# Optimization experiments

Measured on AMD Instinct MI355X. Metric: run time of the kernel, lower is better.

Reference implementation:

```python
import jax, jax.numpy as jnp
import numpy as np

SPATIAL_SHAPES = np.array([[128, 128], [64, 64], [32, 32], [16, 16]], dtype=np.int32)  # (H, W) per level
D_MODEL = 256
D_FFN = 1024
N_LEVELS = 4
N_HEADS = 8
N_POINTS = 4
HEAD_DIM = D_MODEL // N_HEADS
B = 2
LEN = int((SPATIAL_SHAPES[:, 0] * SPATIAL_SHAPES[:, 1]).sum())  # 21760


def layer_norm(x, g, b, eps=1e-5):
    mu = x.mean(-1, keepdims=True)
    var = ((x - mu) ** 2).mean(-1, keepdims=True)
    return (x - mu) / jnp.sqrt(var + eps) * g + b


def ms_deform_attn_core(value, sampling_locations, attention_weights):
    # value: [B, Len, M, D]; locations: [B, Lq, M, L, P, 2] in [0,1]; weights: [B, Lq, M, L, P]
    B_, _, M, D = value.shape
    Lq = sampling_locations.shape[1]
    P = sampling_locations.shape[4]
    out = jnp.zeros((B_, M, Lq, D), value.dtype)
    start = 0
    for lvl, (H, W) in enumerate(SPATIAL_SHAPES.tolist()):
        v = value[:, start:start + H * W].transpose(0, 2, 1, 3)  # [B, M, H*W, D]
        start += H * W
        loc = sampling_locations[:, :, :, lvl].transpose(0, 2, 1, 3, 4)  # [B, M, Lq, P, 2]
        # grid_sample semantics: align_corners=False, padding_mode='zeros'
        x = loc[..., 0] * W - 0.5
        y = loc[..., 1] * H - 0.5
        x0 = jnp.floor(x)
        y0 = jnp.floor(y)
        wx = (x - x0)[..., None]
        wy = (y - y0)[..., None]

        def gather(xi, yi):
            valid = ((xi >= 0) & (xi < W) & (yi >= 0) & (yi < H)).astype(value.dtype)
            idx = (jnp.clip(yi, 0, H - 1) * W + jnp.clip(xi, 0, W - 1)).astype(jnp.int32)
            idx = idx.reshape(B_, M, Lq * P)
            g = jnp.take_along_axis(v, idx[..., None], axis=2).reshape(B_, M, Lq, P, D)
            return g * valid[..., None]

        v00 = gather(x0, y0)
        v01 = gather(x0 + 1, y0)
        v10 = gather(x0, y0 + 1)
        v11 = gather(x0 + 1, y0 + 1)
        samp = (v00 * (1 - wx) + v01 * wx) * (1 - wy) + (v10 * (1 - wx) + v11 * wx) * wy
        w_l = attention_weights[:, :, :, lvl].transpose(0, 2, 1, 3)  # [B, M, Lq, P]
        out = out + (samp * w_l[..., None]).sum(axis=3)
    return out.transpose(0, 2, 1, 3).reshape(B_, Lq, M * D)


def setup_inputs() -> dict:
    key = jax.random.key(0)
    ks = jax.random.split(key, 16)
    f32 = jnp.float32

    def lin(k, fan_in, fan_out, scale=None):
        s = scale if scale is not None else 1.0 / np.sqrt(fan_in)
        return jax.random.normal(k, (fan_in, fan_out), f32) * s

    starts = np.concatenate([[0], np.cumsum(SPATIAL_SHAPES[:, 0] * SPATIAL_SHAPES[:, 1])[:-1]]).astype(np.int32)
    inp = {
        "src": jax.random.normal(ks[0], (B, LEN, D_MODEL), f32),
        "pos": jax.random.normal(ks[1], (B, LEN, D_MODEL), f32),
        "reference_points": jax.random.uniform(ks[2], (B, LEN, N_LEVELS, 2), f32),
        "spatial_shapes": jnp.asarray(SPATIAL_SHAPES),
        "level_start_index": jnp.asarray(starts),
        "norm1_g": jnp.ones((D_MODEL,), f32), "norm1_b": jnp.zeros((D_MODEL,), f32),
        "norm2_g": jnp.ones((D_MODEL,), f32), "norm2_b": jnp.zeros((D_MODEL,), f32),
        "W_value": lin(ks[3], D_MODEL, D_MODEL), "b_value": jnp.zeros((D_MODEL,), f32),
        "W_off": lin(ks[4], D_MODEL, N_HEADS * N_LEVELS * N_POINTS * 2, scale=0.01),
        "b_off": jax.random.normal(ks[5], (N_HEADS * N_LEVELS * N_POINTS * 2,), f32) * 0.01,
        "W_attn": lin(ks[6], D_MODEL, N_HEADS * N_LEVELS * N_POINTS),
        "b_attn": jnp.zeros((N_HEADS * N_LEVELS * N_POINTS,), f32),
        "W_out": lin(ks[7], D_MODEL, D_MODEL), "b_out": jnp.zeros((D_MODEL,), f32),
        "W_ffn1": lin(ks[8], D_MODEL, D_FFN), "b_ffn1": jnp.zeros((D_FFN,), f32),
        "W_ffn2": lin(ks[9], D_FFN, D_MODEL), "b_ffn2": jnp.zeros((D_MODEL,), f32),
    }
    return inp


def reference(src, pos, reference_points, spatial_shapes, level_start_index,
              norm1_g, norm1_b, norm2_g, norm2_b,
              W_value, b_value, W_off, b_off, W_attn, b_attn, W_out, b_out,
              W_ffn1, b_ffn1, W_ffn2, b_ffn2):
    B_, Lq, C = src.shape
    # pre-norm deformable self-attention; NOTE: value path uses un-normed src (faithful to source)
    q = layer_norm(src, norm1_g, norm1_b) + pos
    value = (src @ W_value + b_value).reshape(B_, Lq, N_HEADS, HEAD_DIM)
    offsets = (q @ W_off + b_off).reshape(B_, Lq, N_HEADS, N_LEVELS, N_POINTS, 2)
    attn = jax.nn.softmax((q @ W_attn + b_attn).reshape(B_, Lq, N_HEADS, N_LEVELS * N_POINTS), axis=-1)
    attn = attn.reshape(B_, Lq, N_HEADS, N_LEVELS, N_POINTS)
    offset_normalizer = spatial_shapes[..., ::-1].astype(src.dtype)  # (W, H) per level
    loc = reference_points[:, :, None, :, None, :] + offsets / offset_normalizer[None, None, None, :, None, :]
    attn_out = ms_deform_attn_core(value, loc, attn) @ W_out + b_out
    src = src + attn_out
    h = layer_norm(src, norm2_g, norm2_b)
    h = jax.nn.gelu(h @ W_ffn1 + b_ffn1, approximate=False) @ W_ffn2 + b_ffn2
    return src + h
```

## Files before the change

### kernel.cpp

```cpp
#include <hip/hip_runtime.h>
#include <hip/hip_bf16.h>
#include <math.h>

#define LEN_TOT 21760
#define BATCH 2
#define MROWS (BATCH * LEN_TOT)
#define DMODEL 256
#define DFFN 1024

typedef unsigned short ushort_t;
typedef __attribute__((ext_vector_type(8))) short short8;
typedef __attribute__((ext_vector_type(4))) float floatx4;
typedef __attribute__((address_space(3))) ushort_t lds_us;
typedef __attribute__((address_space(1))) const ushort_t glb_us;

__device__ __forceinline__ ushort_t f2b(float f) {
    unsigned u = __float_as_uint(f);
    unsigned r = (u + 0x7FFFu + ((u >> 16) & 1u)) >> 16;
    return (ushort_t)r;
}

struct TP {
    const float* s[6];
    ushort_t*    d[6];
    int K[6];
    int N[6];
    int start[7];
};

__global__ __launch_bounds__(256) void transpose_convert(TP tp) {
    __shared__ float tile[32][33];
    int blk = blockIdx.x;
    int seg = 0;
    while (seg < 5 && blk >= tp.start[seg + 1]) seg++;
    int local = blk - tp.start[seg];
    int K = tp.K[seg], N = tp.N[seg];
    int tn = N >> 5;
    int k0 = (local / tn) << 5, n0 = (local % tn) << 5;
    int r = threadIdx.x >> 5, c = threadIdx.x & 31;
    const float* src = tp.s[seg];
    #pragma unroll
    for (int rr = r; rr < 32; rr += 8)
        tile[rr][c] = src[(size_t)(k0 + rr) * N + n0 + c];
    __syncthreads();
    ushort_t* dst = tp.d[seg];
    #pragma unroll
    for (int rr = r; rr < 32; rr += 8)
        dst[(size_t)(n0 + rr) * K + k0 + c] = f2b(tile[c][rr]);
}

__global__ void bias_cat(const float* __restrict__ a, const float* __restrict__ b,
                         float* __restrict__ o) {
    int t = threadIdx.x;
    o[t] = (t < 256) ? a[t] : b[t - 256];
}

__global__ __launch_bounds__(256) void ln_dual_kernel(
    const float* __restrict__ x, const float* __restrict__ g,
    const float* __restrict__ bb, const float* __restrict__ addv,
    ushort_t* __restrict__ y_bf, ushort_t* __restrict__ x_bf)
{
    int row  = blockIdx.x * 4 + (threadIdx.x >> 6);
    int lane = threadIdx.x & 63;
    size_t base = (size_t)row * DMODEL + lane * 4;
    float4 v = *(const float4*)(x + base);

    float s = v.x + v.y + v.z + v.w;
    #pragma unroll
    for (int o = 32; o; o >>= 1) s += __shfl_xor(s, o, 64);
    float mu = s * (1.0f / 256.0f);

    float d0 = v.x - mu, d1 = v.y - mu, d2 = v.z - mu, d3 = v.w - mu;
    float vs = d0*d0 + d1*d1 + d2*d2 + d3*d3;
    #pragma unroll
    for (int o = 32; o; o >>= 1) vs += __shfl_xor(vs, o, 64);
    float rstd = rsqrtf(vs * (1.0f / 256.0f) + 1e-5f);

    float4 gv = *(const float4*)(g  + lane * 4);
    float4 bv = *(const float4*)(bb + lane * 4);
    float o0 = d0 * rstd * gv.x + bv.x;
    float o1 = d1 * rstd * gv.y + bv.y;
    float o2 = d2 * rstd * gv.z + bv.z;
    float o3 = d3 * rstd * gv.w + bv.w;
    if (addv) {
        float4 av = *(const float4*)(addv + base);
        o0 += av.x; o1 += av.y; o2 += av.z; o3 += av.w;
    }
    ushort4 ob = {f2b(o0), f2b(o1), f2b(o2), f2b(o3)};
    *(ushort4*)(y_bf + base) = ob;
    if (x_bf) {
        ushort4 xb = {f2b(v.x), f2b(v.y), f2b(v.z), f2b(v.w)};
        *(ushort4*)(x_bf + base) = xb;
    }
}

template<int GELU_ACT, int HAS_RES, int OUT_BF16>
__global__ __launch_bounds__(256) void gemm_mfma(
    const ushort_t* __restrict__ A, const ushort_t* __restrict__ Bt,
    const float* __restrict__ bias, const float* __restrict__ res,
    float* __restrict__ C, ushort_t* __restrict__ Cbf,
    int M, int N, int K)
{
    constexpr int BM = 128, BK = 64;
    __shared__ __align__(16) ushort_t As[BM * BK];
    __shared__ __align__(16) ushort_t Bs[BM * BK];

    const int tid  = threadIdx.x;
    const int wave = tid >> 6;
    const int lane = tid & 63;
    const int wm = (wave & 1) * 64;
    const int wn = (wave >> 1) * 64;
    const int ml = lane & 15;
    const int quad = lane >> 4;
    const int m0 = blockIdx.y * BM, n0 = blockIdx.x * BM;
    const int swz = ml & 7;

    floatx4 acc[4][4] = {};

    for (int k0 = 0; k0 < K; k0 += BK) {
        #pragma unroll
        for (int p = 0; p < 4; p++) {
            int c = p * 256 + tid;
            int r = c >> 3, sp = c & 7;
            int sl = sp ^ (r & 7);
            __builtin_amdgcn_global_load_lds(
                (glb_us*)(A + (size_t)(m0 + r) * K + k0 + sl * 8),
                (lds_us*)(As + c * 8), 16, 0, 0);
            __builtin_amdgcn_global_load_lds(
                (glb_us*)(Bt + (size_t)(n0 + r) * K + k0 + sl * 8),
                (lds_us*)(Bs + c * 8), 16, 0, 0);
        }
        __syncthreads();

        #pragma unroll
        for (int kb = 0; kb < 2; kb++) {
            const int sA = quad + 4 * kb;
            short8 af[4], bfr[4];
            #pragma unroll
            for (int i = 0; i < 4; i++)
                af[i] = *(const short8*)(As + (wm + i * 16 + ml) * BK + (sA ^ swz) * 8);
            #pragma unroll
            for (int j = 0; j < 4; j++)
                bfr[j] = *(const short8*)(Bs + (wn + j * 16 + ml) * BK + (sA ^ swz) * 8);
            #pragma unroll
            for (int i = 0; i < 4; i++)
                #pragma unroll
                for (int j = 0; j < 4; j++)
                    acc[i][j] = __builtin_amdgcn_mfma_f32_16x16x32_bf16(
                        af[i], bfr[j], acc[i][j], 0, 0, 0);
        }
        __syncthreads();
    }

    if (OUT_BF16) {
        ushort_t* pool  = (wave < 2) ? As : Bs;
        ushort_t* wbase = pool + (wave & 1) * 2048;
        const int lr  = lane >> 2;
        const int sg  = lane & 3;
        #pragma unroll
        for (int i = 0; i < 4; i++) {
            ushort_t* wbuf = wbase + (i & 1) * 1024;
            #pragma unroll
            for (int j = 0; j < 4; j++) {
                float bc = bias[n0 + wn + j * 16 + ml];
                #pragma unroll
                for (int r = 0; r < 4; r++) {
                    float v = acc[i][j][r] + bc;
                    if (GELU_ACT) v = 0.5f * v * (1.0f + erff(v * 0.7071067811865476f));
                    if (HAS_RES)
                        v += res[(size_t)(m0 + wm + i * 16 + quad * 4 + r) * N
                                 + n0 + wn + j * 16 + ml];
                    wbuf[(quad * 4 + r) * 64 + j * 16 + ml] = f2b(v);
                }
            }
            asm volatile("s_waitcnt lgkmcnt(0)" ::: "memory");
            #pragma unroll
            for (int h = 0; h < 2; h++) {
                short8 vv = *(const short8*)(wbuf + lr * 64 + (sg + 4 * h) * 8);
                *(short8*)(Cbf + (size_t)(m0 + wm + i * 16 + lr) * N
                                 + n0 + wn + (sg + 4 * h) * 8) = vv;
            }
        }
    } else {
        #pragma unroll
        for (int j = 0; j < 4; j++) {
            int col = n0 + wn + j * 16 + ml;
            float bc = bias[col];
            #pragma unroll
            for (int i = 0; i < 4; i++) {
                int row = m0 + wm + i * 16 + quad * 4;
                #pragma unroll
                for (int r = 0; r < 4; r++) {
                    float v = acc[i][j][r] + bc;
                    if (GELU_ACT) v = 0.5f * v * (1.0f + erff(v * 0.7071067811865476f));
                    if (HAS_RES) v += res[(size_t)(row + r) * N + col];
                    C[(size_t)(row + r) * N + col] = v;
                }
            }
        }
    }
}

__global__ __launch_bounds__(256) void msdeform_kernel(
    const ushort_t* __restrict__ value, const float* __restrict__ qk,
    const float* __restrict__ refp, ushort_t* __restrict__ out_bf)
{
    __shared__ int2 meta[8][16][4];

    const int t  = threadIdx.x;
    const int bq = blockIdx.x;
    const int b  = (bq >= LEN_TOT) ? 1 : 0;

    if (t < 128) {
        int g = t >> 4, i = t & 15;
        float logit = qk[(size_t)bq * 384 + 256 + g * 16 + i];
        float mx = logit;
        #pragma unroll
        for (int o = 8; o; o >>= 1) mx = fmaxf(mx, __shfl_xor(mx, o, 16));
        float e = __expf(logit - mx);
        float se = e;
        #pragma unroll
        for (int o = 8; o; o >>= 1) se += __shfl_xor(se, o, 16);
        float prob = e / se;

        int lvl = i >> 2;
        int Wl  = 128 >> lvl;
        float Wf = (float)Wl;
        const int ST_[4] = {0, 16384, 20480, 21504};

        float2 off2 = *(const float2*)(qk + (size_t)bq * 384 + g * 32 + i * 2);
        float2 ref2 = ((const float2*)refp)[(size_t)bq * 4 + lvl];
        float xs = fmaf(ref2.x, Wf, off2.x) - 0.5f;
        float ys = fmaf(ref2.y, Wf, off2.y) - 0.5f;
        float xf = floorf(xs), yf = floorf(ys);
        int x0 = (int)xf, y0 = (int)yf;
        float wx = xs - xf, wy = ys - yf;
        float wx1 = 1.0f - wx, wy1 = 1.0f - wy;

        bool vx0 = (x0 >= 0) & (x0 < Wl);
        bool vx1 = (x0 + 1 >= 0) & (x0 + 1 < Wl);
        bool vy0 = (y0 >= 0) & (y0 < Wl);
        bool vy1 = (y0 + 1 >= 0) & (y0 + 1 < Wl);
        int cx0 = min(max(x0, 0), Wl - 1);
        int cx1 = min(max(x0 + 1, 0), Wl - 1);
        int cy0 = min(max(y0, 0), Wl - 1);
        int cy1 = min(max(y0 + 1, 0), Wl - 1);

        int vbase = b * LEN_TOT + ST_[lvl];
        int i00 = (vbase + cy0 * Wl + cx0) * 256 + g * 32;
        int i01 = (vbase + cy0 * Wl + cx1) * 256 + g * 32;
        int i10 = (vbase + cy1 * Wl + cx0) * 256 + g * 32;
        int i11 = (vbase + cy1 * Wl + cx1) * 256 + g * 32;
        float w00 = (vx0 && vy0) ? prob * wx1 * wy1 : 0.0f;
        float w01 = (vx1 && vy0) ? prob * wx  * wy1 : 0.0f;
        float w10 = (vx0 && vy1) ? prob * wx1 * wy  : 0.0f;
        float w11 = (vx1 && vy1) ? prob * wx  * wy  : 0.0f;

        *(int4*)&meta[g][i][0] = make_int4(i00, __float_as_int(w00),
                                           i01, __float_as_int(w01));
        *(int4*)&meta[g][i][2] = make_int4(i10, __float_as_int(w10),
                                           i11, __float_as_int(w11));
    }
    __syncthreads();

    const int g  = t >> 5;
    const int l  = t & 31;
    const int cl = l >> 3;
    const int d4 = l & 7;
    float ax = 0.0f, ay = 0.0f, az = 0.0f, aw = 0.0f;
    #pragma unroll
    for (int s = 0; s < 16; s++) {
        int2 mw = meta[g][s][cl];
        float w = __int_as_float(mw.y);
        uint2 u = *(const uint2*)(value + mw.x + (d4 << 2));
        float f0 = __uint_as_float(u.x << 16);
        float f1 = __uint_as_float(u.x & 0xFFFF0000u);
        float f2 = __uint_as_float(u.y << 16);
        float f3 = __uint_as_float(u.y & 0xFFFF0000u);
        ax = fmaf(w, f0, ax); ay = fmaf(w, f1, ay);
        az = fmaf(w, f2, az); aw = fmaf(w, f3, aw);
    }
    ax += __shfl_xor(ax, 8, 32);  ay += __shfl_xor(ay, 8, 32);
    az += __shfl_xor(az, 8, 32);  aw += __shfl_xor(aw, 8, 32);
    ax += __shfl_xor(ax, 16, 32); ay += __shfl_xor(ay, 16, 32);
    az += __shfl_xor(az, 16, 32); aw += __shfl_xor(aw, 16, 32);

    if (l < 8) {
        ushort4 o = {f2b(ax), f2b(ay), f2b(az), f2b(aw)};
        *(ushort4*)(out_bf + ((size_t)bq * 8 + g) * 32 + (d4 << 2)) = o;
    }
}

extern "C" void kernel_launch(void* const* d_in, const int* in_sizes, int n_in,
                              void* d_out, int out_size, void* d_ws, size_t ws_size,
                              hipStream_t stream)
{
    const float* src  = (const float*)d_in[0];
    const float* pos  = (const float*)d_in[1];
    const float* refp = (const float*)d_in[2];
    const float* n1g = (const float*)d_in[5];
    const float* n1b = (const float*)d_in[6];
    const float* n2g = (const float*)d_in[7];
    const float* n2b = (const float*)d_in[8];
    const float* Wv  = (const float*)d_in[9];
    const float* bv  = (const float*)d_in[10];
    const float* Wof = (const float*)d_in[11];
    const float* bof = (const float*)d_in[12];
    const float* Wat = (const float*)d_in[13];
    const float* bat = (const float*)d_in[14];
    const float* Wo  = (const float*)d_in[15];
    const float* bo  = (const float*)d_in[16];
    const float* Wf1 = (const float*)d_in[17];
    const float* bf1 = (const float*)d_in[18];
    const float* Wf2 = (const float*)d_in[19];
    const float* bf2 = (const float*)d_in[20];
    float* out = (float*)d_out;

    char* ws = (char*)d_ws;
    const int M  = MROWS;
    const int Mc = M / 2;
    const size_t SZ_BF = (size_t)M * 256 * 2;

    ushort_t* q_bf     = (ushort_t*)(ws);
    ushort_t* src_bf   = (ushort_t*)(ws + SZ_BF);
    ushort_t* value_bf = (ushort_t*)(ws + 2 * SZ_BF);
    float*    qkb      = (float*)   (ws + 3 * SZ_BF);
    float*    src2     = (float*)   (ws + 4 * SZ_BF);
    ushort_t* h0_bf    = q_bf;
    ushort_t* sampled  = src_bf;
    ushort_t* h1_bf    = value_bf;
    char* wtp = ws + 3 * SZ_BF + (size_t)M * 384 * 4;
    ushort_t* WvT  = (ushort_t*)(wtp);
    ushort_t* WofT = WvT  + 256 * 256;
    ushort_t* WatT = WofT + 256 * 256;
    ushort_t* WoT  = WatT + 256 * 128;
    ushort_t* Wf1T = WoT  + 256 * 256;
    ushort_t* Wf2T = Wf1T + 256 * 1024;
    float*    bqk  = (float*)(Wf2T + 1024 * 256);

    TP tp;
    tp.s[0] = Wv;  tp.d[0] = WvT;  tp.K[0] = 256;  tp.N[0] = 256;
    tp.s[1] = Wof; tp.d[1] = WofT; tp.K[1] = 256;  tp.N[1] = 256;
    tp.s[2] = Wat; tp.d[2] = WatT; tp.K[2] = 256;  tp.N[2] = 128;
    tp.s[3] = Wo;  tp.d[3] = WoT;  tp.K[3] = 256;  tp.N[3] = 256;
    tp.s[4] = Wf1; tp.d[4] = Wf1T; tp.K[4] = 256;  tp.N[4] = 1024;
    tp.s[5] = Wf2; tp.d[5] = Wf2T; tp.K[5] = 1024; tp.N[5] = 256;
    tp.start[0] = 0;   tp.start[1] = 64;  tp.start[2] = 128;
    tp.start[3] = 160; tp.start[4] = 224; tp.start[5] = 480; tp.start[6] = 736;
    transpose_convert<<<736, 256, 0, stream>>>(tp);
    bias_cat<<<1, 384, 0, stream>>>(bof, bat, bqk);

    ln_dual_kernel<<<M / 4, 256, 0, stream>>>(src, n1g, n1b, pos, q_bf, src_bf);
    gemm_mfma<0, 0, 1><<<dim3(2, M / 128), 256, 0, stream>>>(
        src_bf, WvT, bv, nullptr, nullptr, value_bf, M, 256, 256);
    gemm_mfma<0, 0, 0><<<dim3(3, M / 128), 256, 0, stream>>>(
        q_bf, WofT, bqk, nullptr, qkb, nullptr, M, 384, 256);
    msdeform_kernel<<<M, 256, 0, stream>>>(value_bf, qkb, refp, sampled);
    gemm_mfma<0, 1, 0><<<dim3(2, M / 128), 256, 0, stream>>>(
        sampled, WoT, bo, src, src2, nullptr, M, 256, 256);
    ln_dual_kernel<<<M / 4, 256, 0, stream>>>(src2, n2g, n2b, nullptr, h0_bf, nullptr);
    for (int c = 0; c < 2; c++) {
        const ushort_t* h0c = h0_bf + (size_t)c * Mc * 256;
        const float*    s2c = src2  + (size_t)c * Mc * 256;
        float*          oc  = out   + (size_t)c * Mc * 256;
        gemm_mfma<1, 0, 1><<<dim3(8, Mc / 128), 256, 0, stream>>>(
            h0c, Wf1T, bf1, nullptr, nullptr, h1_bf, Mc, 1024, 256);
        gemm_mfma<0, 1, 0><<<dim3(2, Mc / 128), 256, 0, stream>>>(
            h1_bf, Wf2T, bf2, s2c, oc, nullptr, Mc, 256, 1024);
    }
}
```

Measured before the change: 505.4 us.

## Load GEMM fragments directly from global memory and process two queries per deform block

```diff
diff --git a/kernel.cpp b/kernel.cpp
--- a/kernel.cpp
+++ b/kernel.cpp
@@ -11,8 +11,6 @@
 typedef unsigned short ushort_t;
 typedef __attribute__((ext_vector_type(8))) short short8;
 typedef __attribute__((ext_vector_type(4))) float floatx4;
-typedef __attribute__((address_space(3))) ushort_t lds_us;
-typedef __attribute__((address_space(1))) const ushort_t glb_us;
 
 __device__ __forceinline__ ushort_t f2b(float f) {
     unsigned u = __float_as_uint(f);
@@ -95,15 +93,13 @@
 }
 
 template<int GELU_ACT, int HAS_RES, int OUT_BF16>
-__global__ __launch_bounds__(256) void gemm_mfma(
+__global__ __launch_bounds__(256) void gemm_reg(
     const ushort_t* __restrict__ A, const ushort_t* __restrict__ Bt,
     const float* __restrict__ bias, const float* __restrict__ res,
     float* __restrict__ C, ushort_t* __restrict__ Cbf,
     int M, int N, int K)
 {
-    constexpr int BM = 128, BK = 64;
-    __shared__ __align__(16) ushort_t As[BM * BK];
-    __shared__ __align__(16) ushort_t Bs[BM * BK];
+    __shared__ __align__(16) ushort_t epi[4][2048];
 
     const int tid  = threadIdx.x;
     const int wave = tid >> 6;
@@ -112,49 +108,33 @@
     const int wn = (wave >> 1) * 64;
     const int ml = lane & 15;
     const int quad = lane >> 4;
-    const int m0 = blockIdx.y * BM, n0 = blockIdx.x * BM;
-    const int swz = ml & 7;
+    const int m0 = blockIdx.y * 128, n0 = blockIdx.x * 128;
+
+    const ushort_t* Ar = A  + (size_t)(m0 + wm + ml) * K + quad * 8;
+    const ushort_t* Br = Bt + (size_t)(n0 + wn + ml) * K + quad * 8;
+    const int K32 = K >> 5;
 
     floatx4 acc[4][4] = {};
 
-    for (int k0 = 0; k0 < K; k0 += BK) {
-        #pragma unroll
-        for (int p = 0; p < 4; p++) {
-            int c = p * 256 + tid;
-            int r = c >> 3, sp = c & 7;
-            int sl = sp ^ (r & 7);
-            __builtin_amdgcn_global_load_lds(
-                (glb_us*)(A + (size_t)(m0 + r) * K + k0 + sl * 8),
-                (lds_us*)(As + c * 8), 16, 0, 0);
-            __builtin_amdgcn_global_load_lds(
-                (glb_us*)(Bt + (size_t)(n0 + r) * K + k0 + sl * 8),
-                (lds_us*)(Bs + c * 8), 16, 0, 0);
-        }
-        __syncthreads();
-
-        #pragma unroll
-        for (int kb = 0; kb < 2; kb++) {
-            const int sA = quad + 4 * kb;
-            short8 af[4], bfr[4];
-            #pragma unroll
-            for (int i = 0; i < 4; i++)
-                af[i] = *(const short8*)(As + (wm + i * 16 + ml) * BK + (sA ^ swz) * 8);
+    #pragma unroll 4
+    for (int s = 0; s < K32; ++s) {
+        short8 af[4], bfr[4];
+        #pragma unroll
+        for (int i = 0; i < 4; i++)
+            af[i] = *(const short8*)(Ar + (size_t)i * 16 * K + s * 32);
+        #pragma unroll
+        for (int j = 0; j < 4; j++)
+            bfr[j] = *(const short8*)(Br + (size_t)j * 16 * K + s * 32);
+        #pragma unroll
+        for (int i = 0; i < 4; i++)
             #pragma unroll
             for (int j = 0; j < 4; j++)
-                bfr[j] = *(const short8*)(Bs + (wn + j * 16 + ml) * BK + (sA ^ swz) * 8);
-            #pragma unroll
-            for (int i = 0; i < 4; i++)
-                #pragma unroll
-                for (int j = 0; j < 4; j++)
-                    acc[i][j] = __builtin_amdgcn_mfma_f32_16x16x32_bf16(
-                        af[i], bfr[j], acc[i][j], 0, 0, 0);
-        }
-        __syncthreads();
+                acc[i][j] = __builtin_amdgcn_mfma_f32_16x16x32_bf16(
+                    af[i], bfr[j], acc[i][j], 0, 0, 0);
     }
 
     if (OUT_BF16) {
-        ushort_t* pool  = (wave < 2) ? As : Bs;
-        ushort_t* wbase = pool + (wave & 1) * 2048;
+        ushort_t* wbase = epi[wave];
         const int lr  = lane >> 2;
         const int sg  = lane & 3;
         #pragma unroll
@@ -205,14 +185,15 @@
     const ushort_t* __restrict__ value, const float* __restrict__ qk,
     const float* __restrict__ refp, ushort_t* __restrict__ out_bf)
 {
-    __shared__ int2 meta[8][16][4];
-
-    const int t  = threadIdx.x;
-    const int bq = blockIdx.x;
-    const int b  = (bq >= LEN_TOT) ? 1 : 0;
-
-    if (t < 128) {
-        int g = t >> 4, i = t & 15;
+    __shared__ int2 meta[2][8][16][4];
+
+    const int t   = threadIdx.x;
+    const int bq0 = blockIdx.x * 2;
+
+    {
+        int u = t >> 7, g = (t >> 4) & 7, i = t & 15;
+        int bq = bq0 + u;
+        int b  = (bq >= LEN_TOT) ? 1 : 0;
         float logit = qk[(size_t)bq * 384 + 256 + g * 16 + i];
         float mx = logit;
         #pragma unroll
@@ -256,10 +237,10 @@
         float w10 = (vx0 && vy1) ? prob * wx1 * wy  : 0.0f;
         float w11 = (vx1 && vy1) ? prob * wx  * wy  : 0.0f;
 
-        *(int4*)&meta[g][i][0] = make_int4(i00, __float_as_int(w00),
-                                           i01, __float_as_int(w01));
-        *(int4*)&meta[g][i][2] = make_int4(i10, __float_as_int(w10),
-                                           i11, __float_as_int(w11));
+        *(int4*)&meta[u][g][i][0] = make_int4(i00, __float_as_int(w00),
+                                              i01, __float_as_int(w01));
+        *(int4*)&meta[u][g][i][2] = make_int4(i10, __float_as_int(w10),
+                                              i11, __float_as_int(w11));
     }
     __syncthreads();
 
@@ -267,27 +248,29 @@
     const int l  = t & 31;
     const int cl = l >> 3;
     const int d4 = l & 7;
-    float ax = 0.0f, ay = 0.0f, az = 0.0f, aw = 0.0f;
-    #pragma unroll
-    for (int s = 0; s < 16; s++) {
-        int2 mw = meta[g][s][cl];
-        float w = __int_as_float(mw.y);
-        uint2 u = *(const uint2*)(value + mw.x + (d4 << 2));
-        float f0 = __uint_as_float(u.x << 16);
-        float f1 = __uint_as_float(u.x & 0xFFFF0000u);
-        float f2 = __uint_as_float(u.y << 16);
-        float f3 = __uint_as_float(u.y & 0xFFFF0000u);
-        ax = fmaf(w, f0, ax); ay = fmaf(w, f1, ay);
-        az = fmaf(w, f2, az); aw = fmaf(w, f3, aw);
-    }
-    ax += __shfl_xor(ax, 8, 32);  ay += __shfl_xor(ay, 8, 32);
-    az += __shfl_xor(az, 8, 32);  aw += __shfl_xor(aw, 8, 32);
-    ax += __shfl_xor(ax, 16, 32); ay += __shfl_xor(ay, 16, 32);
-    az += __shfl_xor(az, 16, 32); aw += __shfl_xor(aw, 16, 32);
-
-    if (l < 8) {
-        ushort4 o = {f2b(ax), f2b(ay), f2b(az), f2b(aw)};
-        *(ushort4*)(out_bf + ((size_t)bq * 8 + g) * 32 + (d4 << 2)) = o;
+    #pragma unroll
+    for (int u = 0; u < 2; u++) {
+        float ax = 0.0f, ay = 0.0f, az = 0.0f, aw = 0.0f;
+        #pragma unroll
+        for (int s = 0; s < 16; s++) {
+            int2 mw = meta[u][g][s][cl];
+            float w = __int_as_float(mw.y);
+            uint2 uu = *(const uint2*)(value + mw.x + (d4 << 2));
+            float f0 = __uint_as_float(uu.x << 16);
+            float f1 = __uint_as_float(uu.x & 0xFFFF0000u);
+            float f2 = __uint_as_float(uu.y << 16);
+            float f3 = __uint_as_float(uu.y & 0xFFFF0000u);
+            ax = fmaf(w, f0, ax); ay = fmaf(w, f1, ay);
+            az = fmaf(w, f2, az); aw = fmaf(w, f3, aw);
+        }
+        ax += __shfl_xor(ax, 8, 32);  ay += __shfl_xor(ay, 8, 32);
+        az += __shfl_xor(az, 8, 32);  aw += __shfl_xor(aw, 8, 32);
+        ax += __shfl_xor(ax, 16, 32); ay += __shfl_xor(ay, 16, 32);
+        az += __shfl_xor(az, 16, 32); aw += __shfl_xor(aw, 16, 32);
+        if (l < 8) {
+            ushort4 o = {f2b(ax), f2b(ay), f2b(az), f2b(aw)};
+            *(ushort4*)(out_bf + ((size_t)(bq0 + u) * 8 + g) * 32 + (d4 << 2)) = o;
+        }
     }
 }
 
@@ -351,21 +334,21 @@
     bias_cat<<<1, 384, 0, stream>>>(bof, bat, bqk);
 
     ln_dual_kernel<<<M / 4, 256, 0, stream>>>(src, n1g, n1b, pos, q_bf, src_bf);
-    gemm_mfma<0, 0, 1><<<dim3(2, M / 128), 256, 0, stream>>>(
+    gemm_reg<0, 0, 1><<<dim3(2, M / 128), 256, 0, stream>>>(
         src_bf, WvT, bv, nullptr, nullptr, value_bf, M, 256, 256);
-    gemm_mfma<0, 0, 0><<<dim3(3, M / 128), 256, 0, stream>>>(
+    gemm_reg<0, 0, 0><<<dim3(3, M / 128), 256, 0, stream>>>(
         q_bf, WofT, bqk, nullptr, qkb, nullptr, M, 384, 256);
-    msdeform_kernel<<<M, 256, 0, stream>>>(value_bf, qkb, refp, sampled);
-    gemm_mfma<0, 1, 0><<<dim3(2, M / 128), 256, 0, stream>>>(
+    msdeform_kernel<<<M / 2, 256, 0, stream>>>(value_bf, qkb, refp, sampled);
+    gemm_reg<0, 1, 0><<<dim3(2, M / 128), 256, 0, stream>>>(
         sampled, WoT, bo, src, src2, nullptr, M, 256, 256);
     ln_dual_kernel<<<M / 4, 256, 0, stream>>>(src2, n2g, n2b, nullptr, h0_bf, nullptr);
     for (int c = 0; c < 2; c++) {
         const ushort_t* h0c = h0_bf + (size_t)c * Mc * 256;
         const float*    s2c = src2  + (size_t)c * Mc * 256;
         float*          oc  = out   + (size_t)c * Mc * 256;
-        gemm_mfma<1, 0, 1><<<dim3(8, Mc / 128), 256, 0, stream>>>(
+        gemm_reg<1, 0, 1><<<dim3(8, Mc / 128), 256, 0, stream>>>(
             h0c, Wf1T, bf1, nullptr, nullptr, h1_bf, Mc, 1024, 256);
-        gemm_mfma<0, 1, 0><<<dim3(2, Mc / 128), 256, 0, stream>>>(
+        gemm_reg<0, 1, 0><<<dim3(2, Mc / 128), 256, 0, stream>>>(
             h1_bf, Wf2T, bf2, s2c, oc, nullptr, Mc, 256, 1024);
     }
 }
```

Result: slower. 624.4 us (+23.5%).
